# Kernel optimization log

Measured on AMD Instinct MI355X. Metric: run time of the kernel, lower is better.

The kernel has to match this reference:

```python
import jax, jax.numpy as jnp
import numpy as np

N, M, E, R, D, H, V, G = 50000, 8, 800000, 8, 128, 128, 32000, 64
NEG_SLOPE = 0.2  # PyG RGATConv default negative_slope


def setup_inputs() -> dict:
    rng = np.random.default_rng(0)
    # ragged entity-index lists per node, padded with -1
    lengths = rng.integers(1, M + 1, size=N)
    idx = rng.integers(0, V, size=(N, M))
    valid = np.arange(M)[None, :] < lengths[:, None]
    x_with_pad = jnp.asarray(np.where(valid, idx, -1).astype(np.int32))
    edge_index = jnp.asarray(rng.integers(0, N, size=(2, E)).astype(np.int32))
    edge_type = jnp.asarray(rng.integers(0, R, size=E).astype(np.int32))
    batch = jnp.asarray(np.sort(rng.integers(0, G, size=N)).astype(np.int32))
    ks = jax.random.split(jax.random.key(0), 12)
    s = 0.05
    return {
        'x_with_pad': x_with_pad,
        'edge_index': edge_index,
        'edge_type': edge_type,
        'batch': batch,
        'embedding_weights': jax.random.normal(ks[0], (V, D), jnp.float32),
        'w1': jax.random.normal(ks[1], (R, D, H), jnp.float32) * s,
        'q1': jax.random.normal(ks[2], (H, 1), jnp.float32) * s,
        'k1': jax.random.normal(ks[3], (H, 1), jnp.float32) * s,
        'b1': jnp.zeros((H,), jnp.float32),
        'w2': jax.random.normal(ks[4], (R, H, H), jnp.float32) * s,
        'q2': jax.random.normal(ks[5], (H, 1), jnp.float32) * s,
        'k2': jax.random.normal(ks[6], (H, 1), jnp.float32) * s,
        'b2': jnp.zeros((H,), jnp.float32),
        'lin_w': jax.random.normal(ks[7], (H, H), jnp.float32) * s,
        'lin_b': jnp.zeros((H,), jnp.float32),
        'num_graphs': G,
    }


def _rgat_conv(x, src, dst, edge_type, w, q, k, b, num_nodes):
    # x: [N, F]; w: [R, F, O]. Per-node per-relation projection, then
    # per-edge gather (same math as PyG's bmm(x[j], w[edge_type]), cheaper).
    xw = jnp.einsum('nf,rfo->nro', x, w)          # [N, R, O]
    out_i = xw[dst, edge_type]                    # [E, O]
    out_j = xw[src, edge_type]                    # [E, O]
    logits = jax.nn.leaky_relu(out_i @ q + out_j @ k, NEG_SLOPE)  # [E, 1]
    # segment softmax over destination nodes (heads=1)
    m = jax.ops.segment_max(logits, dst, num_segments=num_nodes)   # [N, 1]
    e = jnp.exp(logits - m[dst])
    denom = jax.ops.segment_sum(e, dst, num_segments=num_nodes)
    alpha = e / denom[dst]
    msg = alpha * out_j                           # [E, O]
    return jax.ops.segment_sum(msg, dst, num_segments=num_nodes) + b


def reference(x_with_pad, edge_index, edge_type, batch, embedding_weights,
              w1, q1, k1, b1, w2, q2, k2, b2, lin_w, lin_b, num_graphs):
    num_nodes = x_with_pad.shape[0]
    # vectorized ragged gather + mean (replaces the python per-node loop)
    mask = x_with_pad >= 0                                        # [N, M]
    safe = jnp.where(mask, x_with_pad, 0)
    feats = embedding_weights[safe]                               # [N, M, D]
    maskf = mask.astype(feats.dtype)
    x = (feats * maskf[..., None]).sum(1) / maskf.sum(1, keepdims=True)
    src, dst = edge_index[0], edge_index[1]
    x = _rgat_conv(x, src, dst, edge_type, w1, q1, k1, b1, num_nodes)
    x = jax.nn.relu(x)
    x = _rgat_conv(x, src, dst, edge_type, w2, q2, k2, b2, num_nodes)
    x = jax.nn.relu(x)
    x = x @ lin_w.T + lin_b
    return jax.ops.segment_sum(x, batch, num_segments=num_graphs)  # [G, H]
```

## Files before the change

kernel.cpp:

```cpp
#include <hip/hip_runtime.h>
#include <hip/hip_bf16.h>
#include <math.h>

#define D 128

typedef __attribute__((ext_vector_type(4))) float f32x4;
typedef __attribute__((ext_vector_type(8))) short bf16x8;

__device__ inline unsigned short f2bf(float f){
  unsigned u = __float_as_uint(f);
  u += 0x7fffu + ((u >> 16) & 1u);
  return (unsigned short)(u >> 16);
}
__device__ inline float wred_sum(float v){
#pragma unroll
  for (int m = 1; m < 64; m <<= 1) v += __shfl_xor(v, m, 64);
  return v;
}
__device__ inline float wred_max(float v){
#pragma unroll
  for (int m = 1; m < 64; m <<= 1) v = fmaxf(v, __shfl_xor(v, m, 64));
  return v;
}

__global__ __launch_bounds__(256) void k_pool(const int* __restrict__ xpad,
    const float* __restrict__ emb, unsigned short* __restrict__ xo, int N, int M){
  int wv = threadIdx.x >> 6, ln = threadIdx.x & 63;
  int n = blockIdx.x * 4 + wv;
  if (n >= N) return;
  const int4* xr = (const int4*)(xpad + n * M);
  int4 ia = xr[0], ib = xr[1];
  int cnt = (ia.x >= 0) + (ia.y >= 0) + (ia.z >= 0) + (ia.w >= 0)
          + (ib.x >= 0) + (ib.y >= 0) + (ib.z >= 0) + (ib.w >= 0);
  float2 acc = {0.f, 0.f};
#define POOL_ONE(idx) if ((idx) >= 0){ \
    float2 v = ((const float2*)(emb + (size_t)(idx) * D))[ln]; \
    acc.x += v.x; acc.y += v.y; }
  POOL_ONE(ia.x) POOL_ONE(ia.y) POOL_ONE(ia.z) POOL_ONE(ia.w)
  POOL_ONE(ib.x) POOL_ONE(ib.y) POOL_ONE(ib.z) POOL_ONE(ib.w)
#undef POOL_ONE
  float inv = 1.f / (float)cnt;
  unsigned u = ((unsigned)f2bf(acc.y * inv) << 16) | f2bf(acc.x * inv);
  *(unsigned*)(xo + (size_t)n * D + 2 * ln) = u;
}

__global__ void k_count(const int* __restrict__ dst, int* __restrict__ cnt, int E){
  int e = blockIdx.x * 256 + threadIdx.x;
  if (e < E) atomicAdd(&cnt[dst[e]], 1);
}

__global__ __launch_bounds__(256) void k_scan_blk(const int* __restrict__ cc,
    int* __restrict__ bsum, int nb){
  __shared__ int sh[256];
  int base = blockIdx.x * 1024 + threadIdx.x * 4;
  int s = 0;
#pragma unroll
  for (int j = 0; j < 4; ++j){
    int i = base + j;
    if (i < nb) s += cc[i];
  }
  sh[threadIdx.x] = s; __syncthreads();
  for (int off = 128; off > 0; off >>= 1){
    if (threadIdx.x < off) sh[threadIdx.x] += sh[threadIdx.x + off];
    __syncthreads();
  }
  if (threadIdx.x == 0) bsum[blockIdx.x] = sh[0];
}

__global__ __launch_bounds__(1024) void k_scan_top(const int* __restrict__ bsum,
    int* __restrict__ boff, int* __restrict__ rp, int nblk, int nb){
  __shared__ int sh[1024];
  int t = threadIdx.x;
  int v = (t < nblk) ? bsum[t] : 0;
  sh[t] = v; __syncthreads();
  for (int off = 1; off < 1024; off <<= 1){
    int a = sh[t];
    int b = (t >= off) ? sh[t - off] : 0;
    __syncthreads();
    sh[t] = a + b;
    __syncthreads();
  }
  if (t < nblk) boff[t] = sh[t] - v;
  if (t == 1023) rp[nb] = sh[1023];
}

__global__ __launch_bounds__(256) void k_scan_fin(int* __restrict__ cc,
    const int* __restrict__ boff, int* __restrict__ rp, int nb){
  __shared__ int sh[256];
  int t = threadIdx.x;
  int base = blockIdx.x * 1024 + t * 4;
  int c[4]; int local = 0;
#pragma unroll
  for (int j = 0; j < 4; ++j){
    int i = base + j;
    c[j] = (i < nb) ? cc[i] : 0;
    local += c[j];
  }
  sh[t] = local; __syncthreads();
  for (int off = 1; off < 256; off <<= 1){
    int a = sh[t];
    int b = (t >= off) ? sh[t - off] : 0;
    __syncthreads();
    sh[t] = a + b;
    __syncthreads();
  }
  int run = sh[t] - local + boff[blockIdx.x];
#pragma unroll
  for (int j = 0; j < 4; ++j){
    int i = base + j;
    if (i < nb){ rp[i] = run; cc[i] = run; run += c[j]; }
  }
}

__global__ void k_initcur(const int* __restrict__ rp, int* __restrict__ coarse_cur, int NBk){
  int b = threadIdx.x;
  if (b < NBk) coarse_cur[b] = rp[b * 256];
}

__global__ __launch_bounds__(256) void k_binA(const int* __restrict__ src,
    const int* __restrict__ dst, const int* __restrict__ et,
    int* __restrict__ coarse_cur, int2* __restrict__ tmp, int E){
  __shared__ int lcnt[256], lscan[256], loff[256], gbase[256];
  __shared__ int2 stage[2048];
  __shared__ int staddr[2048];
  int t = threadIdx.x;
  int e0 = blockIdx.x * 2048;
  lcnt[t] = 0; loff[t] = 0;
  __syncthreads();
  int word[8], dd[8], cb[8]; bool val[8];
#pragma unroll
  for (int j = 0; j < 8; ++j){
    int e = e0 + t + j * 256;
    val[j] = (e < E);
    if (val[j]){
      dd[j] = dst[e];
      word[j] = (et[e] << 27) | src[e];
      cb[j] = dd[j] >> 8;
      atomicAdd(&lcnt[cb[j]], 1);
    }
  }
  __syncthreads();
  int v = lcnt[t];
  lscan[t] = v; __syncthreads();
  for (int off = 1; off < 256; off <<= 1){
    int a = lscan[t];
    int b = (t >= off) ? lscan[t - off] : 0;
    __syncthreads();
    lscan[t] = a + b;
    __syncthreads();
  }
  int excl = lscan[t] - v;
  if (v > 0) gbase[t] = atomicAdd(&coarse_cur[t], v);
  lscan[t] = excl;
  __syncthreads();
#pragma unroll
  for (int j = 0; j < 8; ++j){
    if (val[j]){
      int k = atomicAdd(&loff[cb[j]], 1);
      int s = lscan[cb[j]] + k;
      stage[s]  = make_int2(word[j], dd[j]);
      staddr[s] = gbase[cb[j]] + k;
    }
  }
  __syncthreads();
  int tot = lscan[255] + lcnt[255];
  for (int s = t; s < tot; s += 256){
    tmp[staddr[s]] = stage[s];
  }
}

__global__ __launch_bounds__(256) void k_binB(const int* __restrict__ rp,
    const int2* __restrict__ tmp, int* __restrict__ pack, int N){
  __shared__ int lcur[256];
  int nbase = blockIdx.x * 256;
  int nend = nbase + 256; if (nend > N) nend = N;
  int ebeg = rp[nbase], eend = rp[nend];
  lcur[threadIdx.x] = 0;
  __syncthreads();
  for (int i = ebeg + threadIdx.x; i < eend; i += 256){
    int2 v = tmp[i];
    int k = atomicAdd(&lcur[v.y - nbase], 1);
    pack[rp[v.y] + k] = v.x;
  }
}

__global__ void k_wtr(const float* __restrict__ w, unsigned short* __restrict__ wbf, int total){
  int id = blockIdx.x * 256 + threadIdx.x;
  if (id >= total) return;
  int d = id & 127, h = (id >> 7) & 127, r = id >> 14;
  wbf[id] = f2bf(w[(size_t)r * 16384 + d * 128 + h]);
}

__global__ void k_cvt(const float* __restrict__ s, unsigned short* __restrict__ dd, int total){
  int id = blockIdx.x * 256 + threadIdx.x;
  if (id < total) dd[id] = f2bf(s[id]);
}

__global__ __launch_bounds__(256) void k_xw(const unsigned short* __restrict__ x,
    const unsigned short* __restrict__ wbf,
    const float* __restrict__ qv, const float* __restrict__ kv,
    unsigned short* __restrict__ xw,
    float* __restrict__ aT, float* __restrict__ bT,
    int N, int R, int nwg){
  __shared__ __align__(16) char smem[32768];
  unsigned short (*wt)[128] = (unsigned short (*)[128])smem;
  unsigned short (*ot)[136] = (unsigned short (*)[136])smem;
  int wv = threadIdx.x >> 6, ln = threadIdx.x & 63;
  int g = ln >> 4, m16 = ln & 15;
  int orig = blockIdx.x;
  int q = nwg >> 3, rm = nwg & 7;
  int xcd = orig & 7, idx = orig >> 3;
  int wgid = (xcd < rm ? xcd * (q + 1) : rm * (q + 1) + (xcd - rm) * q) + idx;
  int r    = wgid % 8;
  int tile = wgid / 8;
  int n0 = tile * 64;
  int nA = n0 + wv * 16 + m16;
  {
    const uint4* wsrc = (const uint4*)(wbf + (size_t)r * 16384);
    for (int i = threadIdx.x; i < 2048; i += 256){
      int h = i >> 4, c = i & 15;
      *(uint4*)&wt[h][(c ^ (h & 15)) * 8] = wsrc[i];
    }
  }
  bf16x8 af[4];
#pragma unroll
  for (int kc = 0; kc < 4; ++kc) af[kc] = (bf16x8){0,0,0,0,0,0,0,0};
  if (nA < N){
#pragma unroll
    for (int kc = 0; kc < 4; ++kc)
      af[kc] = *(const bf16x8*)(x + (size_t)nA * D + kc * 32 + g * 8);
  }
  __syncthreads();
  f32x4 acc[8];
#pragma unroll
  for (int i = 0; i < 8; ++i) acc[i] = (f32x4){0.f, 0.f, 0.f, 0.f};
#pragma unroll
  for (int kc = 0; kc < 4; ++kc){
#pragma unroll
    for (int hf = 0; hf < 8; ++hf){
      bf16x8 bfr = *(const bf16x8*)&wt[hf * 16 + m16][((kc * 4 + g) ^ m16) * 8];
      acc[hf] = __builtin_amdgcn_mfma_f32_16x16x32_bf16(af[kc], bfr, acc[hf], 0, 0, 0);
    }
  }
  {
    float qr[8], kr[8];
#pragma unroll
    for (int hf = 0; hf < 8; ++hf){ qr[hf] = qv[hf * 16 + m16]; kr[hf] = kv[hf * 16 + m16]; }
#pragma unroll
    for (int jj = 0; jj < 4; ++jj){
      float pa = 0.f, pb = 0.f;
#pragma unroll
      for (int hf = 0; hf < 8; ++hf){
        pa += acc[hf][jj] * qr[hf];
        pb += acc[hf][jj] * kr[hf];
      }
#pragma unroll
      for (int mm = 1; mm < 16; mm <<= 1){
        pa += __shfl_xor(pa, mm, 64);
        pb += __shfl_xor(pb, mm, 64);
      }
      if (m16 == 0){
        int n = n0 + wv * 16 + g * 4 + jj;
        if (n < N){ aT[n * R + r] = pa; bT[n * R + r] = pb; }
      }
    }
  }
  __syncthreads();
#pragma unroll
  for (int hf = 0; hf < 8; ++hf){
#pragma unroll
    for (int jj = 0; jj < 4; ++jj){
      ot[wv * 16 + g * 4 + jj][hf * 16 + m16] = f2bf(acc[hf][jj]);
    }
  }
  __syncthreads();
  unsigned short* dstp = xw + ((size_t)r * N + n0) * 128;
  int limit = (N - n0 < 64) ? (N - n0) * 16 : 1024;
  for (int i = threadIdx.x; i < limit; i += 256){
    int row = i >> 4, c16 = i & 15;
    *(uint4*)(dstp + row * 128 + c16 * 8) = *(const uint4*)&ot[row][c16 * 8];
  }
}

__global__ __launch_bounds__(256) void k_alpha(const int* __restrict__ rp,
    const int* __restrict__ pack, const float* __restrict__ aT, const float* __restrict__ bT,
    float* __restrict__ alp, float* __restrict__ denom, int N, int R){
  int wv = threadIdx.x >> 6, ln = threadIdx.x & 63;
  int n = blockIdx.x * 4 + wv;
  if (n >= N) return;
  int beg = rp[n], end = rp[n + 1];
  if (end <= beg) return;
  float mx = -3.4e38f;
  for (int i = beg + ln; i < end; i += 64){
    int v = pack[i]; int t = v >> 27; int s = v & 0x7ffffff;
    float l = aT[n * R + t] + bT[s * R + t];
    l = l > 0.f ? l : 0.2f * l;
    alp[i] = l;
    mx = fmaxf(mx, l);
  }
  mx = wred_max(mx);
  float sm = 0.f;
  for (int i = beg + ln; i < end; i += 64){
    float ev = __expf(alp[i] - mx);
    alp[i] = ev; sm += ev;
  }
  sm = wred_sum(sm);
  if (ln == 0) denom[n] = 1.f / sm;
}

__global__ __launch_bounds__(256) void k_aggX(const unsigned short* __restrict__ xw,
    const int* __restrict__ rp, const int* __restrict__ pack, const float* __restrict__ alp,
    const float* __restrict__ denom, const float* __restrict__ bias,
    unsigned short* __restrict__ xo, int N, int R){
  int wv = threadIdx.x >> 6, ln = threadIdx.x & 63;
  int n = blockIdx.x * 4 + wv;
  if (n >= N) return;
  int beg = rp[n], end = rp[n + 1];
  float2 s0 = {0.f, 0.f}, s1 = {0.f, 0.f}, s2 = {0.f, 0.f}, s3 = {0.f, 0.f};
  int i = beg;
  for (; i + 3 < end; i += 4){
    int v0 = pack[i], v1 = pack[i + 1], v2 = pack[i + 2], v3 = pack[i + 3];
    float al0 = alp[i], al1 = alp[i + 1], al2 = alp[i + 2], al3 = alp[i + 3];
    unsigned u0 = *(const unsigned*)(xw + ((size_t)(v0 >> 27) * N + (v0 & 0x7ffffff)) * 128 + 2 * ln);
    unsigned u1 = *(const unsigned*)(xw + ((size_t)(v1 >> 27) * N + (v1 & 0x7ffffff)) * 128 + 2 * ln);
    unsigned u2 = *(const unsigned*)(xw + ((size_t)(v2 >> 27) * N + (v2 & 0x7ffffff)) * 128 + 2 * ln);
    unsigned u3 = *(const unsigned*)(xw + ((size_t)(v3 >> 27) * N + (v3 & 0x7ffffff)) * 128 + 2 * ln);
    s0.x += al0 * __uint_as_float(u0 << 16);
    s0.y += al0 * __uint_as_float(u0 & 0xffff0000u);
    s1.x += al1 * __uint_as_float(u1 << 16);
    s1.y += al1 * __uint_as_float(u1 & 0xffff0000u);
    s2.x += al2 * __uint_as_float(u2 << 16);
    s2.y += al2 * __uint_as_float(u2 & 0xffff0000u);
    s3.x += al3 * __uint_as_float(u3 << 16);
    s3.y += al3 * __uint_as_float(u3 & 0xffff0000u);
  }
  for (; i < end; ++i){
    int v0 = pack[i];
    float al0 = alp[i];
    unsigned u0 = *(const unsigned*)(xw + ((size_t)(v0 >> 27) * N + (v0 & 0x7ffffff)) * 128 + 2 * ln);
    s0.x += al0 * __uint_as_float(u0 << 16);
    s0.y += al0 * __uint_as_float(u0 & 0xffff0000u);
  }
  float dn = (end > beg) ? denom[n] : 0.f;
  float ox = fmaxf((s0.x + s1.x + s2.x + s3.x) * dn + bias[2 * ln], 0.f);
  float oy = fmaxf((s0.y + s1.y + s2.y + s3.y) * dn + bias[2 * ln + 1], 0.f);
  unsigned u = ((unsigned)f2bf(oy) << 16) | f2bf(ox);
  *(unsigned*)(xo + (size_t)n * D + 2 * ln) = u;
}

__global__ __launch_bounds__(256) void k_final(const unsigned short* __restrict__ x,
    const unsigned short* __restrict__ lwbf, const float* __restrict__ lb,
    const int* __restrict__ batch, float* __restrict__ out, int N){
  __shared__ unsigned short wt[128][136];
  __shared__ float st[64][129];
  __shared__ int bsh[64];
  {
    const uint4* src = (const uint4*)lwbf;
    for (int i = threadIdx.x; i < 2048; i += 256){
      int h = i >> 4, kblk = i & 15;
      *(uint4*)&wt[h][kblk * 8] = src[i];
    }
  }
  __syncthreads();
  int wv = threadIdx.x >> 6, ln = threadIdx.x & 63;
  int g = ln >> 4, m16 = ln & 15;
  int n0 = blockIdx.x * 64;
  int nA = n0 + wv * 16 + m16;
  f32x4 acc[8];
#pragma unroll
  for (int i = 0; i < 8; ++i) acc[i] = (f32x4){0.f, 0.f, 0.f, 0.f};
#pragma unroll
  for (int kc = 0; kc < 4; ++kc){
    bf16x8 af = (bf16x8){0,0,0,0,0,0,0,0};
    if (nA < N) af = *(const bf16x8*)(x + (size_t)nA * D + kc * 32 + g * 8);
#pragma unroll
    for (int hf = 0; hf < 8; ++hf){
      bf16x8 bfr = *(const bf16x8*)&wt[hf * 16 + m16][kc * 32 + g * 8];
      acc[hf] = __builtin_amdgcn_mfma_f32_16x16x32_bf16(af, bfr, acc[hf], 0, 0, 0);
    }
  }
#pragma unroll
  for (int hf = 0; hf < 8; ++hf){
    int h = hf * 16 + m16;
    float bv = lb[h];
#pragma unroll
    for (int jj = 0; jj < 4; ++jj){
      int row = wv * 16 + g * 4 + jj;
      int n = n0 + row;
      st[row][h] = (n < N) ? (acc[hf][jj] + bv) : 0.f;
    }
  }
  if (threadIdx.x < 64){
    int n = n0 + threadIdx.x;
    bsh[threadIdx.x] = (n < N) ? batch[n] : -1;
  }
  __syncthreads();
  if (threadIdx.x < 128){
    int h = threadIdx.x;
    int lastValid = (N - n0 < 64) ? (N - n0 - 1) : 63;
    int cg = bsh[0];
    float sum = 0.f;
    for (int row = 0; row <= lastValid; ++row){
      int bg = bsh[row];
      if (bg != cg){
        atomicAdd(&out[(size_t)cg * D + h], sum);
        sum = 0.f; cg = bg;
      }
      sum += st[row][h];
    }
    atomicAdd(&out[(size_t)cg * D + h], sum);
  }
}

extern "C" void kernel_launch(void* const* d_in, const int* in_sizes, int n_in,
                              void* d_out, int out_size, void* d_ws, size_t ws_size,
                              hipStream_t stream){
  const int*   xpad  = (const int*)d_in[0];
  const int*   eidx  = (const int*)d_in[1];
  const int*   etyp  = (const int*)d_in[2];
  const int*   batch = (const int*)d_in[3];
  const float* emb   = (const float*)d_in[4];
  const float* w1    = (const float*)d_in[5];
  const float* q1    = (const float*)d_in[6];
  const float* k1    = (const float*)d_in[7];
  const float* b1    = (const float*)d_in[8];
  const float* w2    = (const float*)d_in[9];
  const float* q2    = (const float*)d_in[10];
  const float* k2    = (const float*)d_in[11];
  const float* b2    = (const float*)d_in[12];
  const float* lw    = (const float*)d_in[13];
  const float* lb    = (const float*)d_in[14];

  int N = in_sizes[3];
  int M = in_sizes[0] / N;
  int E = in_sizes[2];
  int R = in_sizes[5] / (128 * 128);
  const int* esrc = eidx;
  const int* edst = eidx + E;

  char* p = (char*)d_ws;
  auto carve = [&](size_t b) -> void* {
    void* q = (void*)p; p += (b + 255) & ~(size_t)255; return q;
  };
  unsigned short* x_a = (unsigned short*)carve((size_t)N * D * 2);
  unsigned short* x_b = (unsigned short*)carve((size_t)N * D * 2);
  float* aT   = (float*)carve((size_t)N * R * 4);
  float* bT   = (float*)carve((size_t)N * R * 4);
  float* dnm  = (float*)carve((size_t)N * 4);
  int*   rp   = (int*)carve((size_t)(N + 1) * 4);
  int*   cur  = (int*)carve((size_t)N * 4);
  int*   pack = (int*)carve((size_t)E * 4);
  float* alp  = (float*)carve((size_t)E * 4);
  int2*  tmp  = (int2*)carve((size_t)E * 8);
  int*   ccur = (int*)carve((size_t)256 * 4);
  unsigned short* wbf1 = (unsigned short*)carve((size_t)R * 128 * 128 * 2);
  unsigned short* wbf2 = (unsigned short*)carve((size_t)R * 128 * 128 * 2);
  unsigned short* lwbf = (unsigned short*)carve((size_t)128 * 128 * 2);
  int* bsum = (int*)carve((size_t)4096 * 4);
  int* boff = (int*)carve((size_t)4096 * 4);
  if ((size_t)(p - (char*)d_ws) > ws_size) return;
  unsigned short* xw = (unsigned short*)carve((size_t)N * R * 128 * 2);
  if ((size_t)(p - (char*)d_ws) > ws_size) return;

  hipMemsetAsync(cur, 0, (size_t)N * 4, stream);
  hipMemsetAsync(d_out, 0, (size_t)out_size * 4, stream);

  int eg = (E + 255) / 256;
  int nblk = (N + 1023) / 1024;
  int NBk = (N + 255) / 256;
  int nbinA = (E + 2047) / 2048;
  k_count   <<<eg, 256, 0, stream>>>(edst, cur, E);
  k_scan_blk<<<nblk, 256, 0, stream>>>(cur, bsum, N);
  k_scan_top<<<1, 1024, 0, stream>>>(bsum, boff, rp, nblk, N);
  k_scan_fin<<<nblk, 256, 0, stream>>>(cur, boff, rp, N);
  k_initcur <<<1, 256, 0, stream>>>(rp, ccur, NBk);
  k_binA    <<<nbinA, 256, 0, stream>>>(esrc, edst, etyp, ccur, tmp, E);
  k_binB    <<<NBk, 256, 0, stream>>>(rp, tmp, pack, N);

  int wtot = R * 128 * 128;
  k_wtr<<<(wtot + 255) / 256, 256, 0, stream>>>(w1, wbf1, wtot);
  k_wtr<<<(wtot + 255) / 256, 256, 0, stream>>>(w2, wbf2, wtot);
  k_cvt<<<(128 * 128 + 255) / 256, 256, 0, stream>>>(lw, lwbf, 128 * 128);

  int ng4 = (N + 3) / 4;
  int ntile = (N + 63) / 64;
  int nwg = ntile * R;
  k_pool<<<ng4, 256, 0, stream>>>(xpad, emb, x_a, N, M);

  k_xw   <<<nwg, 256, 0, stream>>>(x_a, wbf1, q1, k1, xw, aT, bT, N, R, nwg);
  k_alpha<<<ng4, 256, 0, stream>>>(rp, pack, aT, bT, alp, dnm, N, R);
  k_aggX <<<ng4, 256, 0, stream>>>(xw, rp, pack, alp, dnm, b1, x_b, N, R);

  k_xw   <<<nwg, 256, 0, stream>>>(x_b, wbf2, q2, k2, xw, aT, bT, N, R, nwg);
  k_alpha<<<ng4, 256, 0, stream>>>(rp, pack, aT, bT, alp, dnm, N, R);
  k_aggX <<<ng4, 256, 0, stream>>>(xw, rp, pack, alp, dnm, b2, x_a, N, R);

  k_final<<<ntile, 256, 0, stream>>>(x_a, lwbf, lb, batch, (float*)d_out, N);
}
```

Before: 322.6 us.

## Fuse softmax and aggregation into one kernel; widen xw tiles to 128 rows

Merges k_alpha and k_aggX into a single per-node kernel, k_att. It computes the logits and the max, then recomputes the exponentials inside the gather loop and normalises at the end. This removes one launch per layer, the denominator buffer and one write/read pass over the per-edge weights. Separately, k_xw now runs 512 threads over 128-node tiles with slightly more shared memory, halving the workgroup count. Nodes with no edges now write relu(bias) explicitly.

```diff
diff --git a/kernel.cpp b/kernel.cpp
--- a/kernel.cpp
+++ b/kernel.cpp
@@ -11,11 +11,6 @@
   unsigned u = __float_as_uint(f);
   u += 0x7fffu + ((u >> 16) & 1u);
   return (unsigned short)(u >> 16);
-}
-__device__ inline float wred_sum(float v){
-#pragma unroll
-  for (int m = 1; m < 64; m <<= 1) v += __shfl_xor(v, m, 64);
-  return v;
 }
 __device__ inline float wred_max(float v){
 #pragma unroll
@@ -196,13 +191,13 @@
   if (id < total) dd[id] = f2bf(s[id]);
 }
 
-__global__ __launch_bounds__(256) void k_xw(const unsigned short* __restrict__ x,
+__global__ __launch_bounds__(512) void k_xw(const unsigned short* __restrict__ x,
     const unsigned short* __restrict__ wbf,
     const float* __restrict__ qv, const float* __restrict__ kv,
     unsigned short* __restrict__ xw,
     float* __restrict__ aT, float* __restrict__ bT,
     int N, int R, int nwg){
-  __shared__ __align__(16) char smem[32768];
+  __shared__ __align__(16) char smem[34816];
   unsigned short (*wt)[128] = (unsigned short (*)[128])smem;
   unsigned short (*ot)[136] = (unsigned short (*)[136])smem;
   int wv = threadIdx.x >> 6, ln = threadIdx.x & 63;
@@ -213,11 +208,11 @@
   int wgid = (xcd < rm ? xcd * (q + 1) : rm * (q + 1) + (xcd - rm) * q) + idx;
   int r    = wgid % 8;
   int tile = wgid / 8;
-  int n0 = tile * 64;
+  int n0 = tile * 128;
   int nA = n0 + wv * 16 + m16;
   {
     const uint4* wsrc = (const uint4*)(wbf + (size_t)r * 16384);
-    for (int i = threadIdx.x; i < 2048; i += 256){
+    for (int i = threadIdx.x; i < 2048; i += 512){
       int h = i >> 4, c = i & 15;
       *(uint4*)&wt[h][(c ^ (h & 15)) * 8] = wsrc[i];
     }
@@ -275,21 +270,27 @@
   }
   __syncthreads();
   unsigned short* dstp = xw + ((size_t)r * N + n0) * 128;
-  int limit = (N - n0 < 64) ? (N - n0) * 16 : 1024;
-  for (int i = threadIdx.x; i < limit; i += 256){
+  int limit = (N - n0 < 128) ? (N - n0) * 16 : 2048;
+  for (int i = threadIdx.x; i < limit; i += 512){
     int row = i >> 4, c16 = i & 15;
     *(uint4*)(dstp + row * 128 + c16 * 8) = *(const uint4*)&ot[row][c16 * 8];
   }
 }
 
-__global__ __launch_bounds__(256) void k_alpha(const int* __restrict__ rp,
+__global__ __launch_bounds__(256) void k_att(const int* __restrict__ rp,
     const int* __restrict__ pack, const float* __restrict__ aT, const float* __restrict__ bT,
-    float* __restrict__ alp, float* __restrict__ denom, int N, int R){
+    const unsigned short* __restrict__ xw, float* __restrict__ alp,
+    const float* __restrict__ bias, unsigned short* __restrict__ xo, int N, int R){
   int wv = threadIdx.x >> 6, ln = threadIdx.x & 63;
   int n = blockIdx.x * 4 + wv;
   if (n >= N) return;
   int beg = rp[n], end = rp[n + 1];
-  if (end <= beg) return;
+  float bx = bias[2 * ln], by = bias[2 * ln + 1];
+  if (end <= beg){
+    unsigned u = ((unsigned)f2bf(fmaxf(by, 0.f)) << 16) | f2bf(fmaxf(bx, 0.f));
+    *(unsigned*)(xo + (size_t)n * D + 2 * ln) = u;
+    return;
+  }
   float mx = -3.4e38f;
   for (int i = beg + ln; i < end; i += 64){
     int v = pack[i]; int t = v >> 27; int s = v & 0x7ffffff;
@@ -300,50 +301,39 @@
   }
   mx = wred_max(mx);
   float sm = 0.f;
-  for (int i = beg + ln; i < end; i += 64){
-    float ev = __expf(alp[i] - mx);
-    alp[i] = ev; sm += ev;
-  }
-  sm = wred_sum(sm);
-  if (ln == 0) denom[n] = 1.f / sm;
-}
-
-__global__ __launch_bounds__(256) void k_aggX(const unsigned short* __restrict__ xw,
-    const int* __restrict__ rp, const int* __restrict__ pack, const float* __restrict__ alp,
-    const float* __restrict__ denom, const float* __restrict__ bias,
-    unsigned short* __restrict__ xo, int N, int R){
-  int wv = threadIdx.x >> 6, ln = threadIdx.x & 63;
-  int n = blockIdx.x * 4 + wv;
-  if (n >= N) return;
-  int beg = rp[n], end = rp[n + 1];
   float2 s0 = {0.f, 0.f}, s1 = {0.f, 0.f}, s2 = {0.f, 0.f}, s3 = {0.f, 0.f};
   int i = beg;
   for (; i + 3 < end; i += 4){
     int v0 = pack[i], v1 = pack[i + 1], v2 = pack[i + 2], v3 = pack[i + 3];
-    float al0 = alp[i], al1 = alp[i + 1], al2 = alp[i + 2], al3 = alp[i + 3];
+    float e0 = __expf(alp[i]     - mx);
+    float e1 = __expf(alp[i + 1] - mx);
+    float e2 = __expf(alp[i + 2] - mx);
+    float e3 = __expf(alp[i + 3] - mx);
+    sm += e0 + e1 + e2 + e3;
     unsigned u0 = *(const unsigned*)(xw + ((size_t)(v0 >> 27) * N + (v0 & 0x7ffffff)) * 128 + 2 * ln);
     unsigned u1 = *(const unsigned*)(xw + ((size_t)(v1 >> 27) * N + (v1 & 0x7ffffff)) * 128 + 2 * ln);
     unsigned u2 = *(const unsigned*)(xw + ((size_t)(v2 >> 27) * N + (v2 & 0x7ffffff)) * 128 + 2 * ln);
     unsigned u3 = *(const unsigned*)(xw + ((size_t)(v3 >> 27) * N + (v3 & 0x7ffffff)) * 128 + 2 * ln);
-    s0.x += al0 * __uint_as_float(u0 << 16);
-    s0.y += al0 * __uint_as_float(u0 & 0xffff0000u);
-    s1.x += al1 * __uint_as_float(u1 << 16);
-    s1.y += al1 * __uint_as_float(u1 & 0xffff0000u);
-    s2.x += al2 * __uint_as_float(u2 << 16);
-    s2.y += al2 * __uint_as_float(u2 & 0xffff0000u);
-    s3.x += al3 * __uint_as_float(u3 << 16);
-    s3.y += al3 * __uint_as_float(u3 & 0xffff0000u);
+    s0.x += e0 * __uint_as_float(u0 << 16);
+    s0.y += e0 * __uint_as_float(u0 & 0xffff0000u);
+    s1.x += e1 * __uint_as_float(u1 << 16);
+    s1.y += e1 * __uint_as_float(u1 & 0xffff0000u);
+    s2.x += e2 * __uint_as_float(u2 << 16);
+    s2.y += e2 * __uint_as_float(u2 & 0xffff0000u);
+    s3.x += e3 * __uint_as_float(u3 << 16);
+    s3.y += e3 * __uint_as_float(u3 & 0xffff0000u);
   }
   for (; i < end; ++i){
     int v0 = pack[i];
-    float al0 = alp[i];
+    float e0 = __expf(alp[i] - mx);
+    sm += e0;
     unsigned u0 = *(const unsigned*)(xw + ((size_t)(v0 >> 27) * N + (v0 & 0x7ffffff)) * 128 + 2 * ln);
-    s0.x += al0 * __uint_as_float(u0 << 16);
-    s0.y += al0 * __uint_as_float(u0 & 0xffff0000u);
-  }
-  float dn = (end > beg) ? denom[n] : 0.f;
-  float ox = fmaxf((s0.x + s1.x + s2.x + s3.x) * dn + bias[2 * ln], 0.f);
-  float oy = fmaxf((s0.y + s1.y + s2.y + s3.y) * dn + bias[2 * ln + 1], 0.f);
+    s0.x += e0 * __uint_as_float(u0 << 16);
+    s0.y += e0 * __uint_as_float(u0 & 0xffff0000u);
+  }
+  float dn = 1.f / sm;
+  float ox = fmaxf((s0.x + s1.x + s2.x + s3.x) * dn + bx, 0.f);
+  float oy = fmaxf((s0.y + s1.y + s2.y + s3.y) * dn + by, 0.f);
   unsigned u = ((unsigned)f2bf(oy) << 16) | f2bf(ox);
   *(unsigned*)(xo + (size_t)n * D + 2 * ln) = u;
 }
@@ -446,7 +436,6 @@
   unsigned short* x_b = (unsigned short*)carve((size_t)N * D * 2);
   float* aT   = (float*)carve((size_t)N * R * 4);
   float* bT   = (float*)carve((size_t)N * R * 4);
-  float* dnm  = (float*)carve((size_t)N * 4);
   int*   rp   = (int*)carve((size_t)(N + 1) * 4);
   int*   cur  = (int*)carve((size_t)N * 4);
   int*   pack = (int*)carve((size_t)E * 4);
@@ -484,16 +473,15 @@
 
   int ng4 = (N + 3) / 4;
   int ntile = (N + 63) / 64;
-  int nwg = ntile * R;
+  int ntile128 = (N + 127) / 128;
+  int nwg = ntile128 * R;
   k_pool<<<ng4, 256, 0, stream>>>(xpad, emb, x_a, N, M);
 
-  k_xw   <<<nwg, 256, 0, stream>>>(x_a, wbf1, q1, k1, xw, aT, bT, N, R, nwg);
-  k_alpha<<<ng4, 256, 0, stream>>>(rp, pack, aT, bT, alp, dnm, N, R);
-  k_aggX <<<ng4, 256, 0, stream>>>(xw, rp, pack, alp, dnm, b1, x_b, N, R);
-
-  k_xw   <<<nwg, 256, 0, stream>>>(x_b, wbf2, q2, k2, xw, aT, bT, N, R, nwg);
-  k_alpha<<<ng4, 256, 0, stream>>>(rp, pack, aT, bT, alp, dnm, N, R);
-  k_aggX <<<ng4, 256, 0, stream>>>(xw, rp, pack, alp, dnm, b2, x_a, N, R);
+  k_xw <<<nwg, 512, 0, stream>>>(x_a, wbf1, q1, k1, xw, aT, bT, N, R, nwg);
+  k_att<<<ng4, 256, 0, stream>>>(rp, pack, aT, bT, xw, alp, b1, x_b, N, R);
+
+  k_xw <<<nwg, 512, 0, stream>>>(x_b, wbf2, q2, k2, xw, aT, bT, N, R, nwg);
+  k_att<<<ng4, 256, 0, stream>>>(rp, pack, aT, bT, xw, alp, b2, x_a, N, R);
 
   k_final<<<ntile, 256, 0, stream>>>(x_a, lwbf, lb, batch, (float*)d_out, N);
 }
```

After: 295.5 us. -8.4%, faster.
